# Optimization experiments

Hardware: AMD Instinct MI355X
Metric: run time of the kernel (lower is better)

Reference implementation:

```python
import jax, jax.numpy as jnp
import numpy as np

B, N, V, J, K = 2, 16384, 10475, 55, 6
WEIGHT_STD2 = 2.0 * 0.1 ** 2  # 0.02


def setup_inputs() -> dict:
    ks = jax.random.split(jax.random.key(0), 5)
    x = jax.random.normal(ks[0], (B, N, 3), dtype=jnp.float32)
    # cam = [scale, tx, ty]; scale kept positive/near 1
    scale = jax.random.uniform(ks[1], (B, 1), minval=0.8, maxval=1.2)
    trans = jax.random.normal(ks[1], (B, 2)) * 0.05
    cam = jnp.concatenate([scale, trans], axis=-1).astype(jnp.float32)
    # skinning weights: sparse-ish simplex rows
    lbs_weights = jax.nn.softmax(4.0 * jax.random.normal(ks[2], (V, J)), axis=-1).astype(jnp.float32)
    # per-vertex rigid-ish transforms: identity + noise
    verts_transform = (jnp.eye(4, dtype=jnp.float32)[None, None]
                       + 0.1 * jax.random.normal(ks[3], (B, V, 4, 4), dtype=jnp.float32))
    posed_verts = jax.random.normal(ks[4], (B, V, 3), dtype=jnp.float32)
    return {"x": x, "cam": cam, "lbs_weights": lbs_weights,
            "verts_transform": verts_transform, "posed_verts": posed_verts}


def _orth_proj_inv(x, cam):
    # inverse of batch_orth_proj: undo scale, undo xy translation
    scale = cam[:, 0].reshape(-1, 1, 1)
    t = cam[:, 1:3].reshape(-1, 1, 2)
    xy = x[..., :2] / scale - t
    z = x[..., 2:] / scale
    return jnp.concatenate([xy, z], axis=-1)


def _knn(points, verts, k):
    # brute-force KNN on squared euclidean distance (matches knn_points)
    p2 = jnp.sum(points * points, axis=-1, keepdims=True)          # [B,N,1]
    v2 = jnp.sum(verts * verts, axis=-1)                           # [B,V]
    cross = jnp.einsum('bnd,bvd->bnv', points, verts)              # [B,N,V]
    d2 = p2 + v2[:, None, :] - 2.0 * cross
    neg_d, idx = jax.lax.top_k(-d2, k)                             # smallest k
    return jnp.maximum(-neg_d, 0.0), idx


def reference(x, cam, lbs_weights, verts_transform, posed_verts):
    posed_x = _orth_proj_inv(x, cam)                               # [B,N,3]

    # KNN is under torch.no_grad in the original
    dists, idx = _knn(jax.lax.stop_gradient(posed_x),
                      jax.lax.stop_gradient(posed_verts), K)       # [B,N,K]

    # gather skinning weights of neighbors: lbs_weights shared across batch
    w_nb = lbs_weights[idx]                                        # [B,N,K,J]
    conf = jnp.exp(-jnp.sum(jnp.abs(w_nb - w_nb[..., 0:1, :]), axis=-1) / WEIGHT_STD2)
    conf = (conf > 0.9).astype(posed_x.dtype)                      # [B,N,K]

    w = jnp.exp(-dists) * conf
    w = w / jnp.sum(w, axis=-1, keepdims=True)                     # [B,N,K]

    # batched gather of per-vertex transforms
    T_nb = jax.vmap(lambda T, i: T[i])(verts_transform, idx)       # [B,N,K,4,4]
    x_transform = jnp.einsum('bnk,bnkij->bnij', w, T_nb)           # [B,N,4,4]

    # batch_transform: apply rigid transform to posed points
    cano_x = (jnp.einsum('bnij,bnj->bni', x_transform[..., :3, :3], posed_x)
              + x_transform[..., :3, 3])                           # [B,N,3]
    return cano_x
```

## Files before the change

kernel.cpp:

```cpp
#include <hip/hip_runtime.h>
#include <math.h>

#define B_ 2
#define N_ 16384
#define V_ 10475
#define J_ 55
#define K_ 6

constexpr int   NB      = 512;
constexpr int   SSTRIDE = 16384;
constexpr float ZLO     = -6.0f;
constexpr float ZHI     =  6.0f;
constexpr float HBIN    = (ZHI - ZLO) / (float)NB;
constexpr float INVH    = (float)NB / (ZHI - ZLO);

__device__ __forceinline__ int zbin(float z) {
    int b = (int)floorf((z - ZLO) * INVH);
    return min(max(b, 0), NB - 1);
}

__global__ __launch_bounds__(1024) void zero_kernel(int* __restrict__ binCntAll) {
    int i = blockIdx.x * 1024 + threadIdx.x;
    if (i < 2 * B_ * NB) binCntAll[i] = 0;
}

__global__ __launch_bounds__(256) void hist_kernel(const float* __restrict__ pverts,
                                                   const float* __restrict__ x,
                                                   const float* __restrict__ cam,
                                                   int* __restrict__ binCntV,
                                                   int* __restrict__ binCntP) {
    int i = blockIdx.x * 256 + threadIdx.x;
    if (i < B_ * V_) {
        int b = i / V_;
        atomicAdd(&binCntV[b * NB + zbin(pverts[i * 3 + 2])], 1);
    }
    int j = i - B_ * V_;
    if (j >= 0 && j < B_ * N_) {
        int b = j >> 14;
        float z = x[j * 3 + 2] / cam[b * 3 + 0];
        atomicAdd(&binCntP[b * NB + zbin(z)], 1);
    }
}

__global__ __launch_bounds__(NB) void scan_kernel(const int* __restrict__ binCntV,
                                                  const int* __restrict__ binCntP,
                                                  int* __restrict__ binStartV,
                                                  int* __restrict__ binStartP,
                                                  int* __restrict__ binCurV,
                                                  int* __restrict__ binCurP) {
    __shared__ int s[NB];
    int blk = blockIdx.x, t = threadIdx.x;
    const int* cnt;
    int *start, *cur;
    if (blk < 2) { cnt = binCntV + blk * NB; start = binStartV + blk * (NB + 1); cur = binCurV + blk * NB; }
    else         { cnt = binCntP + (blk - 2) * NB; start = binStartP + (blk - 2) * (NB + 1); cur = binCurP + (blk - 2) * NB; }
    int c = cnt[t];
    s[t] = c;
    __syncthreads();
    for (int off = 1; off < NB; off <<= 1) {
        int v = (t >= off) ? s[t - off] : 0;
        __syncthreads();
        s[t] += v;
        __syncthreads();
    }
    int st = s[t] - c;
    start[t] = st;
    cur[t] = st;
    if (t == NB - 1) start[NB] = s[t];
}

__global__ __launch_bounds__(256) void scatter_kernel(const float* __restrict__ pverts,
                                                      const float* __restrict__ x,
                                                      const float* __restrict__ cam,
                                                      int* __restrict__ binCurV,
                                                      int* __restrict__ binCurP,
                                                      float4* __restrict__ pvs,
                                                      int* __restrict__ vidx,
                                                      int* __restrict__ vbin,
                                                      int* __restrict__ psort) {
    int i = blockIdx.x * 256 + threadIdx.x;
    if (i < B_ * V_) {
        int b = i / V_;
        int vi = i - b * V_;
        float vx = pverts[i * 3 + 0], vy = pverts[i * 3 + 1], vz = pverts[i * 3 + 2];
        int bin = zbin(vz);
        int pos = atomicAdd(&binCurV[b * NB + bin], 1);
        pvs[b * SSTRIDE + pos] = make_float4(vx, vy, vz, vx * vx + vy * vy + vz * vz);
        vidx[b * SSTRIDE + pos] = vi;
        vbin[b * SSTRIDE + pos] = bin;
    }
    int j = i - B_ * V_;
    if (j >= 0 && j < B_ * N_) {
        int b = j >> 14;
        float z = x[j * 3 + 2] / cam[b * 3 + 0];
        int pos = atomicAdd(&binCurP[b * NB + zbin(z)], 1);
        psort[b * N_ + pos] = j;
    }
}

__global__ __launch_bounds__(1024, 8) void knn_kernel(const float4* __restrict__ pvs,
                                                      const int* __restrict__ vbin,
                                                      const int* __restrict__ binStartV,
                                                      const int* __restrict__ psort,
                                                      const float* __restrict__ x,
                                                      const float* __restrict__ cam,
                                                      unsigned int* __restrict__ outK) {
    __shared__ float4 tile[2048];
    __shared__ unsigned int cK[16][64][6];
    __shared__ float gateG;

    const int tid = threadIdx.x, lane = tid & 63, wid = tid >> 6;
    const int b   = blockIdx.x >> 8;
    const int blk = blockIdx.x & 255;
    const int pid = psort[b * N_ + blk * 64 + lane];

    const float cs = cam[b * 3 + 0], ctx = cam[b * 3 + 1], cty = cam[b * 3 + 2];
    const float Px = x[pid * 3 + 0] / cs - ctx;
    const float Py = x[pid * 3 + 1] / cs - cty;
    const float Pz = x[pid * 3 + 2] / cs;
    const float Ax = -2.f * Px, Ay = -2.f * Py, Az = -2.f * Pz;
    const float Cc = Px * Px + Py * Py + Pz * Pz + 1.0e-4f;

    float zmin = Pz, zmax = Pz;
#pragma unroll
    for (int m = 1; m <= 32; m <<= 1) {
        zmin = fminf(zmin, __shfl_xor(zmin, m, 64));
        zmax = fmaxf(zmax, __shfl_xor(zmax, m, 64));
    }

    const int* bs = binStartV + b * (NB + 1);
    int cbin = zbin(0.5f * (zmin + zmax));
    int center = (bs[cbin] + bs[cbin + 1]) >> 1;
    int lo = center - 1024;
    lo = max(0, min(lo, V_ - 2048));
    int hi = lo + 2048;

    unsigned int bK[6];
#pragma unroll
    for (int t = 0; t < 6; ++t) bK[t] = 0xFFFFFFFFu;

    const float4* pb = pvs + b * SSTRIDE;
    const int* vbn = vbin + b * SSTRIDE;

#define SCAN_RANGE(RL, CNT)                                                    \
    for (int i = wid; i < (CNT); i += 16) {                                    \
        float4 q = tile[i];                  \
        float d2 = fmaf(Ax, q.x, fmaf(Ay, q.y, fmaf(Az, q.z, Cc + q.w)));      \
        unsigned int key = (__float_as_uint(d2) & 0xFFFFC000u)                 \
                         | (unsigned int)((RL) + i);                           \
        if (key < bK[5]) {                                                     \
            unsigned int kk = key;                                             \
            _Pragma("unroll")                                                  \
            for (int t = 0; t < 6; ++t) {                                      \
                unsigned int mn = min(kk, bK[t]);                              \
                kk = max(kk, bK[t]);                                           \
                bK[t] = mn;                                                    \
            }                                                                  \
        }                                                                      \
    }

    tile[tid]        = pb[lo + tid];
    tile[tid + 1024] = pb[lo + 1024 + tid];
    __syncthreads();
    SCAN_RANGE(lo, 2048)

#pragma unroll
    for (int t = 0; t < 6; ++t) cK[wid][lane][t] = bK[t];
    __syncthreads();
    if (wid == 0) {
        unsigned int U[6];
#pragma unroll
        for (int t = 0; t < 6; ++t) U[t] = 0xFFFFFFFFu;
        for (int ss = 0; ss < 16; ++ss)
#pragma unroll
            for (int t = 0; t < 6; ++t) {
                unsigned int kk = cK[ss][lane][t];
                if (kk < U[5]) {
#pragma unroll
                    for (int u = 0; u < 6; ++u) {
                        unsigned int mn = min(kk, U[u]);
                        kk = max(kk, U[u]);
                        U[u] = mn;
                    }
                }
            }
        float g = __uint_as_float(U[5] | 0x3FFFu);
#pragma unroll
        for (int m = 1; m <= 32; m <<= 1)
            g = fmaxf(g, __shfl_xor(g, m, 64));
        if (lane == 0) gateG = g;
    }
    __syncthreads();
    const float G = gateG;

    while (true) {
        float bl = 3.0e38f, br = 3.0e38f;
        if (lo > 0) {
            int j = __builtin_amdgcn_readfirstlane(vbn[lo - 1]);
            bl = (j >= NB - 1) ? 0.f
               : fmaxf(0.f, zmin - (ZLO + (float)(j + 1) * HBIN));
        }
        if (hi < V_) {
            int j = __builtin_amdgcn_readfirstlane(vbn[hi]);
            br = (j <= 0) ? 0.f
               : fmaxf(0.f, (ZLO + (float)j * HBIN) - zmax);
        }
        bool canL = (lo > 0)  && (bl * bl < G);
        bool canR = (hi < V_) && (br * br < G);
        if (!canL && !canR) break;
        bool left = canL && (!canR || bl <= br);
        int rl, rh;
        if (left) { rh = lo; rl = max(0, lo - 1024); lo = rl; }
        else      { rl = hi; rh = min(V_, hi + 1024); hi = rh; }
        __syncthreads();
        int cnt = rh - rl;
        if (tid < cnt) tile[tid] = pb[rl + tid];
        __syncthreads();
        SCAN_RANGE(rl, cnt)
    }
#undef SCAN_RANGE

    __syncthreads();
#pragma unroll
    for (int t = 0; t < 6; ++t) cK[wid][lane][t] = bK[t];
    __syncthreads();
    if (wid == 0) {
        unsigned int E[8];
#pragma unroll
        for (int t = 0; t < 8; ++t) E[t] = 0xFFFFFFFFu;
        for (int ss = 0; ss < 16; ++ss)
#pragma unroll
            for (int t = 0; t < 6; ++t) {
                unsigned int kk = cK[ss][lane][t];
                if (kk < E[7]) {
#pragma unroll
                    for (int u = 0; u < 8; ++u) {
                        unsigned int mn = min(kk, E[u]);
                        kk = max(kk, E[u]);
                        E[u] = mn;
                    }
                }
            }
#pragma unroll
        for (int t = 0; t < 8; ++t) outK[(size_t)pid * 8 + t] = E[t];
    }
}

__device__ __forceinline__ double shfl_d(double v, int src) {
    int lo = __double2loint(v), hi = __double2hiint(v);
    lo = __shfl(lo, src, 64);
    hi = __shfl(hi, src, 64);
    return __hiloint2double(hi, lo);
}

__global__ __launch_bounds__(256) void epilogue_kernel(const float4* __restrict__ pvs,
                                                       const int* __restrict__ vidx,
                                                       const unsigned int* __restrict__ outK,
                                                       const float* __restrict__ x,
                                                       const float* __restrict__ cam,
                                                       const float* __restrict__ lbs,
                                                       const float* __restrict__ vt,
                                                       float* __restrict__ out) {
    const int lane = threadIdx.x & 63, wid = threadIdx.x >> 6;
    const int p = blockIdx.x * 4 + wid;
    const int b = p >> 14;

    const float cs = cam[b * 3 + 0], ctx = cam[b * 3 + 1], cty = cam[b * 3 + 2];
    const float Px = x[p * 3 + 0] / cs - ctx;
    const float Py = x[p * 3 + 1] / cs - cty;
    const float Pz = x[p * 3 + 2] / cs;

    double myd = 1.0e300;
    int mygi = 0x7FFFFFFF;
    if (lane < 8) {
        unsigned int key = outK[(size_t)p * 8 + lane];
        if (key != 0xFFFFFFFFu) {
            int pos = (int)(key & 0x3FFFu);
            mygi = vidx[b * SSTRIDE + pos];
            float4 vq = pvs[b * SSTRIDE + pos];
            const double csd = (double)cs;
            const double PX = (double)x[p * 3 + 0] / csd - (double)ctx;
            const double PY = (double)x[p * 3 + 1] / csd - (double)cty;
            const double PZ = (double)x[p * 3 + 2] / csd;
            double vx = (double)vq.x, vy = (double)vq.y, vz = (double)vq.z;
            double v2 = vx * vx + vy * vy + vz * vz;
            double P2 = PX * PX + PY * PY + PZ * PZ;
            double dot = PX * vx + PY * vy + PZ * vz;
            myd = P2 + v2 - 2.0 * dot;
        }
    }
    double dd[8];
    int ii[8];
#pragma unroll
    for (int t = 0; t < 8; ++t) { dd[t] = shfl_d(myd, t); ii[t] = __shfl(mygi, t, 64); }
#define CE_(a, c) { \
        bool sw_ = (dd[a] > dd[c]) || (dd[a] == dd[c] && ii[a] > ii[c]); \
        double dt_ = sw_ ? dd[a] : dd[c]; dd[a] = sw_ ? dd[c] : dd[a]; dd[c] = dt_; \
        int it_ = sw_ ? ii[a] : ii[c]; ii[a] = sw_ ? ii[c] : ii[a]; ii[c] = it_; }
#pragma unroll
    for (int r = 0; r < 4; ++r) {
        CE_(0, 1) CE_(2, 3) CE_(4, 5) CE_(6, 7)
        CE_(1, 2) CE_(3, 4) CE_(5, 6)
    }
#undef CE_

    const int i0 = (ii[0] < V_) ? ii[0] : 0;
    float r0v = (lane < J_) ? lbs[i0 * J_ + lane] : 0.f;
    float wgt[K_];
    wgt[0] = expf(-fmaxf((float)dd[0], 0.f));
#pragma unroll
    for (int k = 1; k < K_; ++k) {
        int gk = (ii[k] < V_) ? ii[k] : 0;
        float rkv = (lane < J_) ? lbs[gk * J_ + lane] : 0.f;
        float sv = fabsf(rkv - r0v);
#pragma unroll
        for (int m = 1; m <= 32; m <<= 1) sv += __shfl_xor(sv, m, 64);
        wgt[k] = (sv < 0.0021072103f) ? expf(-fmaxf((float)dd[k], 0.f)) : 0.f;
    }
    float wsum = ((wgt[0] + wgt[1]) + (wgt[2] + wgt[3])) + (wgt[4] + wgt[5]);
    float inv = 1.f / wsum;

    float acc = 0.f;
    if (lane < 16) {
#pragma unroll
        for (int k = 0; k < K_; ++k) {
            int gk = (ii[k] < V_) ? ii[k] : 0;
            acc += (wgt[k] * inv) * vt[((size_t)(b * V_ + gk)) * 16 + lane];
        }
    }
    const int c = lane & 3;
    float pc = (c == 0) ? Px : (c == 1) ? Py : (c == 2) ? Pz : 1.f;
    float part = acc * pc;
    part += __shfl_xor(part, 1, 64);
    part += __shfl_xor(part, 2, 64);
    if (lane == 0)      out[p * 3 + 0] = part;
    else if (lane == 4) out[p * 3 + 1] = part;
    else if (lane == 8) out[p * 3 + 2] = part;
}

extern "C" void kernel_launch(void* const* d_in, const int* in_sizes, int n_in,
                              void* d_out, int out_size, void* d_ws, size_t ws_size,
                              hipStream_t stream) {
    const float* x      = (const float*)d_in[0];
    const float* cam    = (const float*)d_in[1];
    const float* lbs    = (const float*)d_in[2];
    const float* vt     = (const float*)d_in[3];
    const float* pverts = (const float*)d_in[4];
    float* out = (float*)d_out;

    char* ws = (char*)d_ws;
    int* binCntV   = (int*)ws;
    int* binCntP   = binCntV + B_ * NB;
    int* binStartV = binCntP + B_ * NB;
    int* binStartP = binStartV + B_ * (NB + 1);
    int* binCurV   = binStartP + B_ * (NB + 1);
    int* binCurP   = binCurV + B_ * NB;
    char* p16 = (char*)(binCurP + B_ * NB);
    size_t off = ((size_t)(p16 - ws) + 15) & ~(size_t)15;
    float4* pvs = (float4*)(ws + off);
    int* vidx  = (int*)((char*)pvs + (size_t)B_ * SSTRIDE * 16);
    int* vbin  = vidx + B_ * SSTRIDE;
    int* psort = vbin + B_ * SSTRIDE;
    unsigned int* outK = (unsigned int*)(psort + B_ * N_);

    const int histTotal = B_ * V_ + B_ * N_;
    zero_kernel<<<2, 1024, 0, stream>>>(binCntV);
    hist_kernel<<<(histTotal + 255) / 256, 256, 0, stream>>>(pverts, x, cam, binCntV, binCntP);
    scan_kernel<<<4, NB, 0, stream>>>(binCntV, binCntP, binStartV, binStartP, binCurV, binCurP);
    scatter_kernel<<<(histTotal + 255) / 256, 256, 0, stream>>>(pverts, x, cam, binCurV, binCurP,
                                                                pvs, vidx, vbin, psort);
    knn_kernel<<<B_ * (N_ / 64), 1024, 0, stream>>>(pvs, vbin, binStartV, psort, x, cam, outK);
    epilogue_kernel<<<B_ * N_ / 4, 256, 0, stream>>>(pvs, vidx, outK, x, cam, lbs, vt, out);
}
```

Before: 266.7 us.

## Fuse binning pipeline into one shared-memory build kernel and branchless KNN insert

Replaces the zero, histogram, scan and scatter kernels with a single 4-block build kernel that does histogram, prefix scan and scatter in shared memory per batch and kind. This removes three launches and the global atomics. The vbin array is dropped, and the KNN expansion now recomputes the bin from the sorted vertex z. The KNN scan loop also drops the early-out branch in favour of an unconditional sorted insert, unrolled 8 times. The risk is that the build now runs on only 4 blocks, serialising about 27k points per block, and the branchless insert adds ALU work on every candidate.

```diff
diff --git a/kernel.cpp b/kernel.cpp
--- a/kernel.cpp
+++ b/kernel.cpp
@@ -19,87 +19,66 @@
     return min(max(b, 0), NB - 1);
 }
 
-__global__ __launch_bounds__(1024) void zero_kernel(int* __restrict__ binCntAll) {
-    int i = blockIdx.x * 1024 + threadIdx.x;
-    if (i < 2 * B_ * NB) binCntAll[i] = 0;
-}
-
-__global__ __launch_bounds__(256) void hist_kernel(const float* __restrict__ pverts,
-                                                   const float* __restrict__ x,
-                                                   const float* __restrict__ cam,
-                                                   int* __restrict__ binCntV,
-                                                   int* __restrict__ binCntP) {
-    int i = blockIdx.x * 256 + threadIdx.x;
-    if (i < B_ * V_) {
-        int b = i / V_;
-        atomicAdd(&binCntV[b * NB + zbin(pverts[i * 3 + 2])], 1);
-    }
-    int j = i - B_ * V_;
-    if (j >= 0 && j < B_ * N_) {
-        int b = j >> 14;
-        float z = x[j * 3 + 2] / cam[b * 3 + 0];
-        atomicAdd(&binCntP[b * NB + zbin(z)], 1);
-    }
-}
-
-__global__ __launch_bounds__(NB) void scan_kernel(const int* __restrict__ binCntV,
-                                                  const int* __restrict__ binCntP,
-                                                  int* __restrict__ binStartV,
-                                                  int* __restrict__ binStartP,
-                                                  int* __restrict__ binCurV,
-                                                  int* __restrict__ binCurP) {
-    __shared__ int s[NB];
-    int blk = blockIdx.x, t = threadIdx.x;
-    const int* cnt;
-    int *start, *cur;
-    if (blk < 2) { cnt = binCntV + blk * NB; start = binStartV + blk * (NB + 1); cur = binCurV + blk * NB; }
-    else         { cnt = binCntP + (blk - 2) * NB; start = binStartP + (blk - 2) * (NB + 1); cur = binCurP + (blk - 2) * NB; }
-    int c = cnt[t];
-    s[t] = c;
-    __syncthreads();
+__global__ __launch_bounds__(1024) void build_kernel(const float* __restrict__ pverts,
+                                                     const float* __restrict__ x,
+                                                     const float* __restrict__ cam,
+                                                     float4* __restrict__ pvs,
+                                                     int* __restrict__ vidx,
+                                                     int* __restrict__ psort,
+                                                     int* __restrict__ binStartV) {
+    __shared__ int hist[NB];
+    __shared__ int cur[NB];
+    const int t = threadIdx.x;
+    const int b = blockIdx.x >> 1;
+    const bool vertsKind = (blockIdx.x & 1) == 0;
+
+    if (t < NB) hist[t] = 0;
+    __syncthreads();
+
+    if (vertsKind) {
+        for (int i = t; i < V_; i += 1024)
+            atomicAdd(&hist[zbin(pverts[((size_t)(b * V_ + i)) * 3 + 2])], 1);
+    } else {
+        const float cs = cam[b * 3 + 0];
+        for (int i = t; i < N_; i += 1024)
+            atomicAdd(&hist[zbin(x[((size_t)(b * N_ + i)) * 3 + 2] / cs)], 1);
+    }
+    __syncthreads();
+
     for (int off = 1; off < NB; off <<= 1) {
-        int v = (t >= off) ? s[t - off] : 0;
+        int v = 0;
+        if (t < NB && t >= off) v = hist[t - off];
         __syncthreads();
-        s[t] += v;
+        if (t < NB) hist[t] += v;
         __syncthreads();
     }
-    int st = s[t] - c;
-    start[t] = st;
-    cur[t] = st;
-    if (t == NB - 1) start[NB] = s[t];
-}
-
-__global__ __launch_bounds__(256) void scatter_kernel(const float* __restrict__ pverts,
-                                                      const float* __restrict__ x,
-                                                      const float* __restrict__ cam,
-                                                      int* __restrict__ binCurV,
-                                                      int* __restrict__ binCurP,
-                                                      float4* __restrict__ pvs,
-                                                      int* __restrict__ vidx,
-                                                      int* __restrict__ vbin,
-                                                      int* __restrict__ psort) {
-    int i = blockIdx.x * 256 + threadIdx.x;
-    if (i < B_ * V_) {
-        int b = i / V_;
-        int vi = i - b * V_;
-        float vx = pverts[i * 3 + 0], vy = pverts[i * 3 + 1], vz = pverts[i * 3 + 2];
-        int bin = zbin(vz);
-        int pos = atomicAdd(&binCurV[b * NB + bin], 1);
-        pvs[b * SSTRIDE + pos] = make_float4(vx, vy, vz, vx * vx + vy * vy + vz * vz);
-        vidx[b * SSTRIDE + pos] = vi;
-        vbin[b * SSTRIDE + pos] = bin;
-    }
-    int j = i - B_ * V_;
-    if (j >= 0 && j < B_ * N_) {
-        int b = j >> 14;
-        float z = x[j * 3 + 2] / cam[b * 3 + 0];
-        int pos = atomicAdd(&binCurP[b * NB + zbin(z)], 1);
-        psort[b * N_ + pos] = j;
+    if (t < NB) {
+        int ex = (t == 0) ? 0 : hist[t - 1];
+        cur[t] = ex;
+        if (vertsKind) binStartV[b * (NB + 1) + t] = ex;
+    }
+    if (vertsKind && t == 0) binStartV[b * (NB + 1) + NB] = hist[NB - 1];
+    __syncthreads();
+
+    if (vertsKind) {
+        for (int i = t; i < V_; i += 1024) {
+            size_t g = (size_t)(b * V_ + i) * 3;
+            float vx = pverts[g], vy = pverts[g + 1], vz = pverts[g + 2];
+            int pos = atomicAdd(&cur[zbin(vz)], 1);
+            pvs[b * SSTRIDE + pos] = make_float4(vx, vy, vz, vx * vx + vy * vy + vz * vz);
+            vidx[b * SSTRIDE + pos] = i;
+        }
+    } else {
+        const float cs = cam[b * 3 + 0];
+        for (int i = t; i < N_; i += 1024) {
+            float z = x[((size_t)(b * N_ + i)) * 3 + 2] / cs;
+            int pos = atomicAdd(&cur[zbin(z)], 1);
+            psort[b * N_ + pos] = b * N_ + i;
+        }
     }
 }
 
 __global__ __launch_bounds__(1024, 8) void knn_kernel(const float4* __restrict__ pvs,
-                                                      const int* __restrict__ vbin,
                                                       const int* __restrict__ binStartV,
                                                       const int* __restrict__ psort,
                                                       const float* __restrict__ x,
@@ -140,22 +119,19 @@
     for (int t = 0; t < 6; ++t) bK[t] = 0xFFFFFFFFu;
 
     const float4* pb = pvs + b * SSTRIDE;
-    const int* vbn = vbin + b * SSTRIDE;
 
 #define SCAN_RANGE(RL, CNT)                                                    \
+    _Pragma("unroll 8")                                                        \
     for (int i = wid; i < (CNT); i += 16) {                                    \
         float4 q = tile[i];                  \
         float d2 = fmaf(Ax, q.x, fmaf(Ay, q.y, fmaf(Az, q.z, Cc + q.w)));      \
-        unsigned int key = (__float_as_uint(d2) & 0xFFFFC000u)                 \
-                         | (unsigned int)((RL) + i);                           \
-        if (key < bK[5]) {                                                     \
-            unsigned int kk = key;                                             \
-            _Pragma("unroll")                                                  \
-            for (int t = 0; t < 6; ++t) {                                      \
-                unsigned int mn = min(kk, bK[t]);                              \
-                kk = max(kk, bK[t]);                                           \
-                bK[t] = mn;                                                    \
-            }                                                                  \
+        unsigned int kk = (__float_as_uint(d2) & 0xFFFFC000u)                  \
+                        | (unsigned int)((RL) + i);                            \
+        _Pragma("unroll")                                                      \
+        for (int t = 0; t < 6; ++t) {                                          \
+            unsigned int mn = min(kk, bK[t]);                                  \
+            kk = max(kk, bK[t]);                                               \
+            bK[t] = mn;                                                        \
         }                                                                      \
     }
 
@@ -196,12 +172,12 @@
     while (true) {
         float bl = 3.0e38f, br = 3.0e38f;
         if (lo > 0) {
-            int j = __builtin_amdgcn_readfirstlane(vbn[lo - 1]);
+            int j = zbin(pb[lo - 1].z);
             bl = (j >= NB - 1) ? 0.f
                : fmaxf(0.f, zmin - (ZLO + (float)(j + 1) * HBIN));
         }
         if (hi < V_) {
-            int j = __builtin_amdgcn_readfirstlane(vbn[hi]);
+            int j = zbin(pb[hi].z);
             br = (j <= 0) ? 0.f
                : fmaxf(0.f, (ZLO + (float)j * HBIN) - zmax);
         }
@@ -349,26 +325,13 @@
     float* out = (float*)d_out;
 
     char* ws = (char*)d_ws;
-    int* binCntV   = (int*)ws;
-    int* binCntP   = binCntV + B_ * NB;
-    int* binStartV = binCntP + B_ * NB;
-    int* binStartP = binStartV + B_ * (NB + 1);
-    int* binCurV   = binStartP + B_ * (NB + 1);
-    int* binCurP   = binCurV + B_ * NB;
-    char* p16 = (char*)(binCurP + B_ * NB);
-    size_t off = ((size_t)(p16 - ws) + 15) & ~(size_t)15;
-    float4* pvs = (float4*)(ws + off);
+    int* binStartV = (int*)ws;
+    float4* pvs = (float4*)(ws + 4112);
     int* vidx  = (int*)((char*)pvs + (size_t)B_ * SSTRIDE * 16);
-    int* vbin  = vidx + B_ * SSTRIDE;
-    int* psort = vbin + B_ * SSTRIDE;
+    int* psort = vidx + B_ * SSTRIDE;
     unsigned int* outK = (unsigned int*)(psort + B_ * N_);
 
-    const int histTotal = B_ * V_ + B_ * N_;
-    zero_kernel<<<2, 1024, 0, stream>>>(binCntV);
-    hist_kernel<<<(histTotal + 255) / 256, 256, 0, stream>>>(pverts, x, cam, binCntV, binCntP);
-    scan_kernel<<<4, NB, 0, stream>>>(binCntV, binCntP, binStartV, binStartP, binCurV, binCurP);
-    scatter_kernel<<<(histTotal + 255) / 256, 256, 0, stream>>>(pverts, x, cam, binCurV, binCurP,
-                                                                pvs, vidx, vbin, psort);
-    knn_kernel<<<B_ * (N_ / 64), 1024, 0, stream>>>(pvs, vbin, binStartV, psort, x, cam, outK);
+    build_kernel<<<4, 1024, 0, stream>>>(pverts, x, cam, pvs, vidx, psort, binStartV);
+    knn_kernel<<<B_ * (N_ / 64), 1024, 0, stream>>>(pvs, binStartV, psort, x, cam, outK);
     epilogue_kernel<<<B_ * N_ / 4, 256, 0, stream>>>(pvs, vidx, outK, x, cam, lbs, vt, out);
 }
```

New measurement: 271.4 us. No clear change (+1.8%).
